# Optimization experiments

Measured on AMD Instinct MI355X. Metric: run time of the kernel, lower is better.

Reference implementation:

```python
import jax, jax.numpy as jnp
import numpy as np

# dims: batch, input channels, hidden neurons, actions, time bins
B, C_IN, HID, OUT, T = 1024, 8, 300, 2, 300
TS, TAU_SR, THETA = 1.0, 10.0, 10.0   # simulation step, SRM kernel tau, spike threshold
TAU_REF, SCALE_REF = 2.0, 2.0          # refractory alpha-kernel tau and scale
TAU_RHO, SCALE_RHO = 1.0, 1.0          # surrogate-gradient pdf params (SLAYER)
K = 100                                 # SRM kernel truncation length (alpha kernel is negligible past 10*tau)

_t = np.arange(K, dtype=np.float32) * TS
SRM = jnp.asarray((_t / TAU_SR) * np.exp(1.0 - _t / TAU_SR))  # alpha PSP kernel, eps(0)=0


def psp(x):
    # slayer.psp: causal temporal convolution of the weighted input with the SRM alpha kernel. x: [B, C, T]
    b, c, t = x.shape
    lhs = x.reshape(b * c, 1, t)
    rhs = SRM[::-1].reshape(1, 1, K).astype(x.dtype)  # flip so correlation == causal convolution
    out = jax.lax.conv_general_dilated(lhs, rhs, (1,), [(K - 1, 0)],
                                       dimension_numbers=('NCH', 'OIH', 'NCH'))
    return out.reshape(b, c, t)


@jax.custom_vjp
def heaviside(u):
    # forward: hard threshold; backward: SLAYER surrogate pdf scaleRho/tauRho * exp(-|u|/tauRho)
    return (u >= 0).astype(u.dtype)

def _hs_fwd(u):
    return heaviside(u), u

def _hs_bwd(u, g):
    return (g * (SCALE_RHO / TAU_RHO) * jnp.exp(-jnp.abs(u) / TAU_RHO),)

heaviside.defvjp(_hs_fwd, _hs_bwd)


def spike(u):
    # slayer.spike: integrate-and-fire with an alpha-shaped refractory response
    # refKernel(n) = -scaleRef*theta * (n*Ts/tauRef) * exp(1 - n*Ts/tauRef)
    # realized exactly via a 2-state linear recurrence (x = n*a^n term, y = a^n term)
    a = jnp.exp(jnp.asarray(-TS / TAU_REF, u.dtype))
    A = jnp.asarray(-SCALE_REF * THETA * np.e * TS / TAU_REF, u.dtype)

    def step(carry, u_t):
        x, y = carry                     # x: accumulated refractory potential at this step
        s = heaviside(u_t + x - THETA)   # membrane (psp + refractory) vs threshold
        y2 = y + A * s                   # spike injects impulse into the alpha-kernel state
        return (a * (x + y2), a * y2), s

    u_tbc = jnp.moveaxis(u, -1, 0)  # [T, B, C]
    z = jnp.zeros(u.shape[:-1], u.dtype)
    _, s = jax.lax.scan(step, (z, z), u_tbc)
    return jnp.moveaxis(s, 0, -1)


def setup_inputs():
    key = jax.random.key(0)
    k1, k2, k3 = jax.random.split(key, 3)
    # CartPoleEncoder output is a spike train: Bernoulli(0.3) spikes over T bins
    encoded_input = (jax.random.uniform(k1, (B, C_IN, T)) < 0.3).astype(jnp.float32)
    W1 = jax.random.normal(k2, (HID, C_IN), dtype=jnp.float32)
    W2 = jax.random.normal(k3, (OUT, HID), dtype=jnp.float32)
    return {"encoded_input": encoded_input, "W1": W1, "W2": W2}


def reference(encoded_input, W1, W2):
    # fc is a 1x1x1 conv3d == per-timestep dense layer over channels
    sl1 = spike(psp(jnp.einsum('bit,oi->bot', encoded_input, W1)))  # [B, 300, T]
    sl2 = spike(psp(jnp.einsum('bht,oh->bot', sl1, W2)))            # [B, 2, T]
    logits = jnp.sum(sl2, axis=-1)                                   # spike counts -> Categorical logits [B, 2]
    g = jax.random.gumbel(jax.random.key(42), logits.shape, logits.dtype)
    pi = jnp.argmax(logits + g, axis=-1)                             # Categorical sample via Gumbel-max
    logp = jax.nn.log_softmax(logits, axis=-1)
    logp_pi = jnp.take_along_axis(logp, pi[:, None], axis=-1)[:, 0]
    return logits, pi, logp_pi
```

## Files before the change

kernel.cpp:

```cpp
#include <hip/hip_runtime.h>
#include <stdint.h>


#define NB    1024
#define CIN   8
#define HID   300
#define TLEN  300
#define KTAP  99
#define THETA 10.0f

#define LDS_K1 134144

typedef float f4 __attribute__((ext_vector_type(4)));

__device__ __forceinline__ void threefry2x32(uint32_t c0, uint32_t c1,
                                             uint32_t& o0, uint32_t& o1) {
  const uint32_t k0 = 0u, k1 = 42u;
  const uint32_t k2 = k0 ^ k1 ^ 0x1BD11BDAu;
  uint32_t x0 = c0 + k0, x1 = c1 + k1;
#define TFR(r) { x0 += x1; x1 = (x1 << (r)) | (x1 >> (32 - (r))); x1 ^= x0; }
  TFR(13) TFR(15) TFR(26) TFR(6)  x0 += k1; x1 += k2 + 1u;
  TFR(17) TFR(29) TFR(16) TFR(24) x0 += k2; x1 += k0 + 2u;
  TFR(13) TFR(15) TFR(26) TFR(6)  x0 += k0; x1 += k1 + 3u;
  TFR(17) TFR(29) TFR(16) TFR(24) x0 += k1; x1 += k2 + 4u;
  TFR(13) TFR(15) TFR(26) TFR(6)  x0 += k2; x1 += k0 + 5u;
#undef TFR
  o0 = x0; o1 = x1;
}

__device__ __forceinline__ float jax_uniform_from_bits(uint32_t bits) {
  uint32_t fb = (bits >> 9) | 0x3F800000u;
  float f = __uint_as_float(fb) - 1.0f;
  const float tiny = 1.17549435e-38f;
  float u = __fadd_rn(f, tiny);
  return fmaxf(tiny, u);
}

__global__ void snn_taps_kernel(double* __restrict__ tapsG) {
  const int i = threadIdx.x;
  if (i < 107) {
    const int j = i - 2;
    double v = 0.0;
    if (j >= 1 && j <= KTAP) {
      float q  = (float)j / 10.0f;
      float ef = (float)exp((double)(1.0f - q));
      v = (double)__fmul_rn(q, ef);
    }
    tapsG[i] = v;
  }
}

__global__ __launch_bounds__(320)
void snn_enc_kernel(const float* __restrict__ enc, uint32_t* __restrict__ encBG) {
  const int b = blockIdx.x, t = threadIdx.x;
  if (t < TLEN) {
    uint32_t m = 0u;
#pragma unroll
    for (int c = 0; c < CIN; ++c)
      if (enc[b * (CIN * TLEN) + c * TLEN + t] != 0.0f) m |= (1u << c);
    encBG[b * TLEN + t] = m;
  }
}

__global__ __launch_bounds__(1024, 1)
void snn_l1_kernel(const float* __restrict__ W1,
                   const double* __restrict__ tapsG,
                   const uint32_t* __restrict__ encBG,
                   unsigned long long* __restrict__ maskG) {
  extern __shared__ char smem[];
  float* xq   = (float*)(smem);
  f4*    xqv  = (f4*)(smem);
  float* ubuf = (float*)(smem + 103424);

  const int tid  = threadIdx.x;
  const int lane = tid & 63;
  const int wv   = tid >> 6;
  const int bh   = blockIdx.x;
  const int b    = blockIdx.y;
  const int h    = bh * 64 + lane;

  for (int i = tid; i < 101 * 64; i += 1024)
    xqv[i] = (f4)(0.0f);
  __syncthreads();

  float w1f[8];
#pragma unroll
  for (int c = 0; c < 8; ++c)
    w1f[c] = (h < HID) ? W1[h * 8 + c] : 0.0f;

  for (int t = wv; t < TLEN; t += 16) {
    const uint32_t bits = encBG[__builtin_amdgcn_readfirstlane(b * TLEN + t)];
    float xf = 0.0f;
#pragma unroll
    for (int c = 0; c < 8; ++c) {
      float wsel = (bits & (1u << c)) ? w1f[c] : 0.0f;
      xf = __fadd_rn(xf, wsel);
    }
    const int slot = 101 + t;
    xq[(slot >> 2) * 256 + lane * 4 + (slot & 3)] = xf;
  }
  __syncthreads();

  const float arf = (float)0.6065306597126334;
  const float Af  = (float)-27.182818284590452;

  auto fir_chunk = [&](int s, int c, int bufsel) {
    const int t0 = 60 * s + 4 * c;
    double a0 = 0.0, a1 = 0.0, a2 = 0.0, a3 = 0.0;
#pragma clang loop unroll(disable)
    for (int g = 0; g < 13; ++g) {
      const int m0 = __builtin_amdgcn_readfirstlane(g << 3);
      const int qb = (96 + t0 - (g << 3)) >> 2;
      f4 v0 = xqv[qb * 64 + lane];
      f4 v1 = xqv[(qb + 1) * 64 + lane];
      double kt[11];
#pragma unroll
      for (int u = 0; u < 11; ++u) kt[u] = tapsG[m0 + u];
      double x64[8];
#pragma unroll
      for (int u = 0; u < 4; ++u) {
        x64[u]     = (double)v0[u];
        x64[4 + u] = (double)v1[u];
      }
#pragma unroll
      for (int d = 0; d < 8; ++d) {
        const double xv = x64[7 - d];
        a0 += kt[d + 0] * xv;
        a1 += kt[d + 1] * xv;
        a2 += kt[d + 2] * xv;
        a3 += kt[d + 3] * xv;
      }
    }
    float* ub = ubuf + bufsel * (60 * 64) + (4 * c) * 64 + lane;
    ub[0]   = (float)a0;
    ub[64]  = (float)a1;
    ub[128] = (float)a2;
    ub[192] = (float)a3;
  };

  float RX = 0.0f, RY = 0.0f;
  unsigned long long* maskW = maskG + (size_t)b * (5 * TLEN) + bh * TLEN;

  auto scan_stage = [&](int s) {
    const float* ub = ubuf + (s & 1) * (60 * 64) + lane;
#pragma clang loop unroll(disable)
    for (int r = 0; r < 60; r += 4) {
      float u0 = ub[(r + 0) * 64];
      float u1 = ub[(r + 1) * 64];
      float u2 = ub[(r + 2) * 64];
      float u3 = ub[(r + 3) * 64];
#pragma unroll
      for (int d = 0; d < 4; ++d) {
        float umem = (d == 0) ? u0 : (d == 1) ? u1 : (d == 2) ? u2 : u3;
        float v  = __fsub_rn(__fadd_rn(umem, RX), THETA);
        bool  sp = (v >= 0.0f) && (h < HID);
        unsigned long long bal = __ballot(sp);
        if (lane == 0) maskW[60 * s + r + d] = bal;
        float sf = sp ? 1.0f : 0.0f;
        float y2 = __fadd_rn(RY, __fmul_rn(Af, sf));
        RX = __fmul_rn(arf, __fadd_rn(RX, y2));
        RY = __fmul_rn(arf, y2);
      }
    }
  };

  if (wv < 15) fir_chunk(0, wv, 0);
  __syncthreads();
#pragma clang loop unroll(disable)
  for (int s = 0; s < 5; ++s) {
    if (wv == 0)      scan_stage(s);
    else if (s < 4)   fir_chunk(s + 1, wv - 1, (s + 1) & 1);
    __syncthreads();
  }
}

__global__ __launch_bounds__(320)
void snn_l2_kernel(const float* __restrict__ W2,
                   const unsigned long long* __restrict__ maskG,
                   float* __restrict__ out) {
  __shared__ double             kD[100];
  __shared__ double             W2D[2 * HID];
  __shared__ unsigned long long maskL[5 * TLEN];
  __shared__ double             zD[2 * 304];
  __shared__ float              u2L[2 * 304];
  __shared__ float              lgL[2];

  const int tid = threadIdx.x;
  const int b   = blockIdx.x;

  const float arf = (float)0.6065306597126334;
  const float Af  = (float)-27.182818284590452;

  for (int j = tid; j < 100; j += 320) {
    float q  = (float)j / 10.0f;
    float ef = (float)exp((double)(1.0f - q));
    kD[j] = (double)__fmul_rn(q, ef);
  }
  for (int i = tid; i < 2 * HID; i += 320)
    W2D[i] = (double)W2[i];
  for (int i = tid; i < 5 * TLEN; i += 320)
    maskL[i] = maskG[(size_t)b * (5 * TLEN) + i];
  __syncthreads();

  if (tid < TLEN) {
    const int t = tid;
    double z0 = 0.0, z1 = 0.0;
#pragma unroll
    for (int w5 = 0; w5 < 5; ++w5) {
      const unsigned long long mm = maskL[w5 * TLEN + t];
      const int kend = (w5 == 4) ? (HID - 256) : 64;
      for (int k = 0; k < kend; ++k) {
        const bool bit = (mm >> k) & 1ull;
        const int  hh  = w5 * 64 + k;
        z0 += bit ? W2D[hh] : 0.0;
        z1 += bit ? W2D[HID + hh] : 0.0;
      }
    }
    zD[t]       = (double)((float)z0);
    zD[304 + t] = (double)((float)z1);
  }
  __syncthreads();

  if (tid < TLEN) {
    const int t = tid;
    double a0 = 0.0, a1 = 0.0;
    const int jmax = (t < KTAP) ? t : KTAP;
    for (int j = 1; j <= jmax; ++j) {
      const double kk = kD[j];
      a0 += kk * zD[t - j];
      a1 += kk * zD[304 + t - j];
    }
    u2L[t]       = (float)a0;
    u2L[304 + t] = (float)a1;
  }
  __syncthreads();

  if (tid < 2) {
    float RX = 0.0f, RY = 0.0f;
    int cnt = 0;
    for (int t = 0; t < TLEN; ++t) {
      float u  = u2L[tid * 304 + t];
      float v  = __fsub_rn(__fadd_rn(u, RX), THETA);
      bool  sp = (v >= 0.0f);
      cnt += sp ? 1 : 0;
      float sf = sp ? 1.0f : 0.0f;
      float y2 = __fadd_rn(RY, __fmul_rn(Af, sf));
      RX = __fmul_rn(arf, __fadd_rn(RX, y2));
      RY = __fmul_rn(arf, y2);
    }
    lgL[tid] = (float)cnt;
  }
  __syncthreads();

  if (tid == 0) {
    float l0 = lgL[0], l1 = lgL[1];
    uint32_t o0, o1;
    threefry2x32(0u, 2u * (uint32_t)b, o0, o1);
    float g0 = -logf(-logf(jax_uniform_from_bits(o0 ^ o1)));
    threefry2x32(0u, 2u * (uint32_t)b + 1u, o0, o1);
    float g1 = -logf(-logf(jax_uniform_from_bits(o0 ^ o1)));

    float v0 = __fadd_rn(l0, g0);
    float v1 = __fadd_rn(l1, g1);
    int   pi = (v1 > v0) ? 1 : 0;
    float m   = fmaxf(l0, l1);
    float s0f = __fsub_rn(l0, m), s1f = __fsub_rn(l1, m);
    float lse = logf(__fadd_rn(expf(s0f), expf(s1f)));
    float lp  = __fsub_rn(pi ? s1f : s0f, lse);

    out[2 * b + 0] = l0;
    out[2 * b + 1] = l1;
    out[2048 + b]  = (float)pi;
    out[3072 + b]  = lp;
  }
}

extern "C" void kernel_launch(void* const* d_in, const int* in_sizes, int n_in,
                              void* d_out, int out_size, void* d_ws, size_t ws_size,
                              hipStream_t stream) {
  const float* enc = (const float*)d_in[0];
  const float* W1  = (const float*)d_in[1];
  const float* W2  = (const float*)d_in[2];
  float* out = (float*)d_out;

  double*             tapsG = (double*)d_ws;
  uint32_t*           encBG = (uint32_t*)((char*)d_ws + 1024);
  unsigned long long* maskG = (unsigned long long*)((char*)d_ws + 1024 + 1228800);

  hipFuncSetAttribute((const void*)snn_l1_kernel,
                      hipFuncAttributeMaxDynamicSharedMemorySize, LDS_K1);

  snn_taps_kernel<<<dim3(1), dim3(128), 0, stream>>>(tapsG);
  snn_enc_kernel<<<dim3(NB), dim3(320), 0, stream>>>(enc, encBG);
  snn_l1_kernel<<<dim3(5, NB), dim3(1024), LDS_K1, stream>>>(W1, tapsG, encBG, maskG);
  snn_l2_kernel<<<dim3(NB), dim3(320), 0, stream>>>(W2, maskG, out);
}
```

Baseline: 799.4 us.

## Widen FIR register tile to 8 outputs with double-buffered tap/input loads

The layer-1 FIR chunk now computes 8 output timesteps per wave instead of 4, loading 16 inputs and vectorized double-pair taps per group. Tap and input loads for the next group are software-pipelined with sched_barriers. Stages become 56 steps (six in total, the last only 20), so fewer FIR waves run per stage. The input staging now writes whole f4 vectors with zero padding inline, which removes the separate LDS clearing pass. The aim is more FMA work per loaded tap and LDS read, hiding load latency. In exchange it raises register pressure and adds an extra scan stage serialized on wave 0.

```diff
diff --git a/kernel.cpp b/kernel.cpp
--- a/kernel.cpp
+++ b/kernel.cpp
@@ -9,9 +9,10 @@
 #define KTAP  99
 #define THETA 10.0f
 
-#define LDS_K1 134144
-
-typedef float f4 __attribute__((ext_vector_type(4)));
+#define LDS_K1 133120
+
+typedef float  f4  __attribute__((ext_vector_type(4)));
+typedef double d2v __attribute__((ext_vector_type(2)));
 
 __device__ __forceinline__ void threefry2x32(uint32_t c0, uint32_t c1,
                                              uint32_t& o0, uint32_t& o1) {
@@ -36,17 +37,17 @@
   return fmaxf(tiny, u);
 }
 
-__global__ void snn_taps_kernel(double* __restrict__ tapsG) {
+__global__ void snn_taps_kernel(double* __restrict__ tapsP) {
   const int i = threadIdx.x;
-  if (i < 107) {
-    const int j = i - 2;
+  if (i < 104) {
+    const int j = i + 1;
     double v = 0.0;
-    if (j >= 1 && j <= KTAP) {
+    if (j <= KTAP) {
       float q  = (float)j / 10.0f;
       float ef = (float)exp((double)(1.0f - q));
       v = (double)__fmul_rn(q, ef);
     }
-    tapsG[i] = v;
+    tapsP[i] = v;
   }
 }
 
@@ -64,13 +65,12 @@
 
 __global__ __launch_bounds__(1024, 1)
 void snn_l1_kernel(const float* __restrict__ W1,
-                   const double* __restrict__ tapsG,
+                   const double* __restrict__ tapsP,
                    const uint32_t* __restrict__ encBG,
                    unsigned long long* __restrict__ maskG) {
   extern __shared__ char smem[];
-  float* xq   = (float*)(smem);
   f4*    xqv  = (f4*)(smem);
-  float* ubuf = (float*)(smem + 103424);
+  float* ubuf = (float*)(smem + 104448);
 
   const int tid  = threadIdx.x;
   const int lane = tid & 63;
@@ -79,72 +79,103 @@
   const int b    = blockIdx.y;
   const int h    = bh * 64 + lane;
 
-  for (int i = tid; i < 101 * 64; i += 1024)
-    xqv[i] = (f4)(0.0f);
-  __syncthreads();
+  int vzero;
+  asm volatile("v_mov_b32 %0, 0" : "=v"(vzero));
 
   float w1f[8];
 #pragma unroll
   for (int c = 0; c < 8; ++c)
     w1f[c] = (h < HID) ? W1[h * 8 + c] : 0.0f;
 
-  for (int t = wv; t < TLEN; t += 16) {
-    const uint32_t bits = encBG[__builtin_amdgcn_readfirstlane(b * TLEN + t)];
-    float xf = 0.0f;
-#pragma unroll
-    for (int c = 0; c < 8; ++c) {
-      float wsel = (bits & (1u << c)) ? w1f[c] : 0.0f;
-      xf = __fadd_rn(xf, wsel);
-    }
-    const int slot = 101 + t;
-    xq[(slot >> 2) * 256 + lane * 4 + (slot & 3)] = xf;
+#pragma clang loop unroll(disable)
+  for (int q = wv; q < 102; q += 16) {
+    f4 v;
+#pragma unroll
+    for (int o = 0; o < 4; ++o) {
+      const int t = (q << 2) + o - 104;
+      float xf = 0.0f;
+      if (t >= 0 && t < TLEN) {
+        const uint32_t bits = encBG[__builtin_amdgcn_readfirstlane(b * TLEN + t)];
+#pragma unroll
+        for (int c = 0; c < 8; ++c)
+          xf = __fadd_rn(xf, (bits & (1u << c)) ? w1f[c] : 0.0f);
+      }
+      v[o] = xf;
+    }
+    xqv[q * 64 + lane] = v;
   }
   __syncthreads();
 
   const float arf = (float)0.6065306597126334;
   const float Af  = (float)-27.182818284590452;
 
-  auto fir_chunk = [&](int s, int c, int bufsel) {
-    const int t0 = 60 * s + 4 * c;
-    double a0 = 0.0, a1 = 0.0, a2 = 0.0, a3 = 0.0;
+#define LOADG(g_, x0_, x1_, x2_, x3_, k0_, k1_, k2_, k3_) do {            \
+    const int qb_ = ((t0 - ((g_) << 3) + 96) >> 2) * 64 + lane;           \
+    x0_ = xqv[qb_];        x1_ = xqv[qb_ + 64];                           \
+    x2_ = xqv[qb_ + 128];  x3_ = xqv[qb_ + 192];                          \
+    const d2v* tp_ = (const d2v*)(tapsP) + (((g_) << 2) + vzero);         \
+    k0_ = tp_[0]; k1_ = tp_[1]; k2_ = tp_[2]; k3_ = tp_[3];               \
+  } while (0)
+
+#define FMAG(EMAX, x0_, x1_, x2_, x3_, k0_, k1_, k2_, k3_) do {           \
+    double x64_[16];                                                      \
+    _Pragma("unroll")                                                     \
+    for (int o_ = 0; o_ < 4; ++o_) {                                      \
+      x64_[o_]      = (double)x0_[o_];                                    \
+      x64_[4 + o_]  = (double)x1_[o_];                                    \
+      x64_[8 + o_]  = (double)x2_[o_];                                    \
+      x64_[12 + o_] = (double)x3_[o_];                                    \
+    }                                                                     \
+    double kt_[8];                                                        \
+    kt_[0] = k0_[0]; kt_[1] = k0_[1]; kt_[2] = k1_[0]; kt_[3] = k1_[1];   \
+    kt_[4] = k2_[0]; kt_[5] = k2_[1]; kt_[6] = k3_[0]; kt_[7] = k3_[1];   \
+    _Pragma("unroll")                                                     \
+    for (int e_ = 0; e_ <= (EMAX); ++e_) {                                \
+      const double kk_ = kt_[e_];                                         \
+      _Pragma("unroll")                                                   \
+      for (int i_ = 0; i_ < 8; ++i_)                                      \
+        acc[i_] += kk_ * x64_[i_ - e_ + 7];                               \
+    }                                                                     \
+  } while (0)
+
+  auto fir_chunk = [&](int sbase, int cl, int bufsel) {
+    const int t0 = sbase + (cl << 3);
+    double acc[8];
+#pragma unroll
+    for (int i = 0; i < 8; ++i) acc[i] = 0.0;
+
+    f4  xa0, xa1, xa2, xa3, xb0, xb1, xb2, xb3;
+    d2v ka0, ka1, ka2, ka3, kb0, kb1, kb2, kb3;
+
+    LOADG(0, xa0, xa1, xa2, xa3, ka0, ka1, ka2, ka3);
+    __builtin_amdgcn_sched_barrier(0);
 #pragma clang loop unroll(disable)
-    for (int g = 0; g < 13; ++g) {
-      const int m0 = __builtin_amdgcn_readfirstlane(g << 3);
-      const int qb = (96 + t0 - (g << 3)) >> 2;
-      f4 v0 = xqv[qb * 64 + lane];
-      f4 v1 = xqv[(qb + 1) * 64 + lane];
-      double kt[11];
-#pragma unroll
-      for (int u = 0; u < 11; ++u) kt[u] = tapsG[m0 + u];
-      double x64[8];
-#pragma unroll
-      for (int u = 0; u < 4; ++u) {
-        x64[u]     = (double)v0[u];
-        x64[4 + u] = (double)v1[u];
-      }
-#pragma unroll
-      for (int d = 0; d < 8; ++d) {
-        const double xv = x64[7 - d];
-        a0 += kt[d + 0] * xv;
-        a1 += kt[d + 1] * xv;
-        a2 += kt[d + 2] * xv;
-        a3 += kt[d + 3] * xv;
-      }
-    }
-    float* ub = ubuf + bufsel * (60 * 64) + (4 * c) * 64 + lane;
-    ub[0]   = (float)a0;
-    ub[64]  = (float)a1;
-    ub[128] = (float)a2;
-    ub[192] = (float)a3;
+    for (int g = 0; g < 12; g += 2) {
+      LOADG(g + 1, xb0, xb1, xb2, xb3, kb0, kb1, kb2, kb3);
+      __builtin_amdgcn_sched_barrier(0);
+      FMAG(7, xa0, xa1, xa2, xa3, ka0, ka1, ka2, ka3);
+      __builtin_amdgcn_sched_barrier(0);
+      LOADG(g + 2, xa0, xa1, xa2, xa3, ka0, ka1, ka2, ka3);
+      __builtin_amdgcn_sched_barrier(0);
+      FMAG(7, xb0, xb1, xb2, xb3, kb0, kb1, kb2, kb3);
+      __builtin_amdgcn_sched_barrier(0);
+    }
+    FMAG(2, xa0, xa1, xa2, xa3, ka0, ka1, ka2, ka3);
+
+    float* ub = ubuf + bufsel * (56 * 64) + (cl << 3) * 64 + lane;
+#pragma unroll
+    for (int i = 0; i < 8; ++i)
+      ub[i * 64] = (float)acc[i];
   };
 
   float RX = 0.0f, RY = 0.0f;
   unsigned long long* maskW = maskG + (size_t)b * (5 * TLEN) + bh * TLEN;
 
   auto scan_stage = [&](int s) {
-    const float* ub = ubuf + (s & 1) * (60 * 64) + lane;
+    const int tlen = (s == 5) ? 20 : 56;
+    const float* ub = ubuf + (s & 1) * (56 * 64) + lane;
 #pragma clang loop unroll(disable)
-    for (int r = 0; r < 60; r += 4) {
+    for (int r = 0; r < tlen; r += 4) {
       float u0 = ub[(r + 0) * 64];
       float u1 = ub[(r + 1) * 64];
       float u2 = ub[(r + 2) * 64];
@@ -155,7 +186,7 @@
         float v  = __fsub_rn(__fadd_rn(umem, RX), THETA);
         bool  sp = (v >= 0.0f) && (h < HID);
         unsigned long long bal = __ballot(sp);
-        if (lane == 0) maskW[60 * s + r + d] = bal;
+        if (lane == 0) maskW[56 * s + r + d] = bal;
         float sf = sp ? 1.0f : 0.0f;
         float y2 = __fadd_rn(RY, __fmul_rn(Af, sf));
         RX = __fmul_rn(arf, __fadd_rn(RX, y2));
@@ -164,14 +195,20 @@
     }
   };
 
-  if (wv < 15) fir_chunk(0, wv, 0);
+  if (wv < 7) fir_chunk(0, wv, 0);
   __syncthreads();
 #pragma clang loop unroll(disable)
-  for (int s = 0; s < 5; ++s) {
-    if (wv == 0)      scan_stage(s);
-    else if (s < 4)   fir_chunk(s + 1, wv - 1, (s + 1) & 1);
+  for (int s = 0; s < 6; ++s) {
+    if (wv == 0) {
+      scan_stage(s);
+    } else if (s < 5) {
+      const int nc = (s + 1 == 5) ? 3 : 7;
+      if (wv - 1 < nc) fir_chunk(56 * (s + 1), wv - 1, (s + 1) & 1);
+    }
     __syncthreads();
   }
+#undef LOADG
+#undef FMAG
 }
 
 __global__ __launch_bounds__(320)
@@ -283,15 +320,15 @@
   const float* W2  = (const float*)d_in[2];
   float* out = (float*)d_out;
 
-  double*             tapsG = (double*)d_ws;
+  double*             tapsP = (double*)d_ws;
   uint32_t*           encBG = (uint32_t*)((char*)d_ws + 1024);
   unsigned long long* maskG = (unsigned long long*)((char*)d_ws + 1024 + 1228800);
 
   hipFuncSetAttribute((const void*)snn_l1_kernel,
                       hipFuncAttributeMaxDynamicSharedMemorySize, LDS_K1);
 
-  snn_taps_kernel<<<dim3(1), dim3(128), 0, stream>>>(tapsG);
+  snn_taps_kernel<<<dim3(1), dim3(128), 0, stream>>>(tapsP);
   snn_enc_kernel<<<dim3(NB), dim3(320), 0, stream>>>(enc, encBG);
-  snn_l1_kernel<<<dim3(5, NB), dim3(1024), LDS_K1, stream>>>(W1, tapsG, encBG, maskG);
+  snn_l1_kernel<<<dim3(5, NB), dim3(1024), LDS_K1, stream>>>(W1, tapsP, encBG, maskG);
   snn_l2_kernel<<<dim3(NB), dim3(320), 0, stream>>>(W2, maskG, out);
 }
```

New measurement: 777.3 us. 1.03x faster.
